# Performance work log

Hardware: AMD Instinct MI355X
Metric: run time of the kernel (lower is better)

The kernel has to match this reference:

```python
import jax, jax.numpy as jnp
import numpy as np

N_HEAD = 16
QK_NOPE = 128
QK_ROPE = 64
QK_HEAD = QK_NOPE + QK_ROPE  # 192
V_HEAD = 128
SCALE = 1.0 / np.sqrt(QK_HEAD)


def setup_inputs() -> dict:
    key = jax.random.key(0)
    ks = jax.random.split(key, 8)
    B, T, C = 2, 2048, 2048
    s = lambda fan: 1.0 / np.sqrt(fan)
    return {
        "x": jax.random.normal(ks[0], (B, T, C), jnp.float32),
        "freqs_cis": jax.random.uniform(ks[1], (T, QK_ROPE // 2, 2), jnp.float32),
        "w_q": jax.random.normal(ks[2], (C, N_HEAD * QK_HEAD), jnp.float32) * s(C),
        "w_kv_down": jax.random.normal(ks[3], (C, 256), jnp.float32) * s(C),
        "w_k_up": jax.random.normal(ks[4], (256, N_HEAD * QK_HEAD), jnp.float32) * s(256),
        "w_v_up": jax.random.normal(ks[5], (256, N_HEAD * V_HEAD), jnp.float32) * s(256),
        "w_o": jax.random.normal(ks[6], (N_HEAD * V_HEAD, C), jnp.float32) * s(N_HEAD * V_HEAD),
        "start_pos": 0,
    }


def _rotate_half(x):
    x1, x2 = x[..., : x.shape[-1] // 2], x[..., x.shape[-1] // 2 :]
    return jnp.concatenate([-x2, x1], axis=-1)


def reference(x, freqs_cis, w_q, w_kv_down, w_k_up, w_v_up, w_o, start_pos):
    B, T, C = x.shape
    # low-rank MLA projections
    q = (x @ w_q).reshape(B, T, N_HEAD, QK_HEAD)
    kv = x @ w_kv_down                                  # (B,T,r)
    k = (kv @ w_k_up).reshape(B, T, N_HEAD, QK_HEAD)
    v = (kv @ w_v_up).reshape(B, T, N_HEAD, V_HEAD)

    # inline RoPE on decoupled rope dims
    q_nope, q_rope = q[..., :QK_NOPE], q[..., QK_NOPE:]
    k_nope, k_rope = k[..., :QK_NOPE], k[..., QK_NOPE:]
    freqs = freqs_cis[start_pos : start_pos + T]         # (T, 32, 2)
    cos = freqs[..., 0][None, :, None, :]                # (1,T,1,32)
    sin = freqs[..., 1][None, :, None, :]
    rep = QK_ROPE // cos.shape[-1]
    cos = jnp.tile(cos, (1, 1, 1, rep))                  # (1,T,1,64)
    sin = jnp.tile(sin, (1, 1, 1, rep))
    q_rope = q_rope * cos + _rotate_half(q_rope) * sin
    k_rope = k_rope * cos + _rotate_half(k_rope) * sin
    q = jnp.concatenate([q_nope, q_rope], axis=-1)
    k = jnp.concatenate([k_nope, k_rope], axis=-1)

    # causal SDPA with mismatched QK vs V head dims
    scores = jnp.einsum("bqhd,bkhd->bhqk", q, k) * SCALE
    causal = jnp.tril(jnp.ones((T, T), dtype=bool))
    scores = jnp.where(causal[None, None], scores, -jnp.inf)
    probs = jax.nn.softmax(scores, axis=-1)
    out = jnp.einsum("bhqk,bkhd->bqhd", probs, v)        # (B,T,H,V_HEAD)
    out = out.reshape(B, T, N_HEAD * V_HEAD)
    return out @ w_o
```

## Files before the change

kernel.cpp:

```cpp
#include <hip/hip_runtime.h>
#include <stdint.h>

typedef unsigned short u16;
typedef float f32x4 __attribute__((ext_vector_type(4)));
typedef __bf16 bf16x8 __attribute__((ext_vector_type(8)));

static __device__ __forceinline__ u16 f2bf(float f) {
  union { float f; unsigned u; } v; v.f = f;
  unsigned r = v.u + 0x7fffu + ((v.u >> 16) & 1u);
  return (u16)(r >> 16);
}
static __device__ __forceinline__ float bf2f(u16 h) {
  union { unsigned u; float f; } v; v.u = ((unsigned)h) << 16;
  return v.f;
}

#define GLD_LDS16(gp, lp) __builtin_amdgcn_global_load_lds( \
    (__attribute__((address_space(1))) void*)(gp),          \
    (__attribute__((address_space(3))) void*)(lp), 16, 0, 0)

#define MFMA16(a, b, c) __builtin_amdgcn_mfma_f32_16x16x32_bf16((a), (b), (c), 0, 0, 0)

__global__ void conv_bf16_kernel(const float* __restrict__ in, u16* __restrict__ out, long n) {
  long stride = (long)gridDim.x * blockDim.x * 4;
  for (long i = ((long)blockIdx.x * blockDim.x + threadIdx.x) * 4; i < n; i += stride) {
    float4 v = *(const float4*)(in + i);
    union { u16 s[4]; uint2 u; } pk;
    pk.s[0] = f2bf(v.x); pk.s[1] = f2bf(v.y); pk.s[2] = f2bf(v.z); pk.s[3] = f2bf(v.w);
    *(uint2*)(out + i) = pk.u;
  }
}

__global__ void transpose_conv_kernel(const float* __restrict__ W, u16* __restrict__ WT,
                                      int K, int N) {
  __shared__ float tile[32][33];
  const int n0 = blockIdx.x * 32, k0 = blockIdx.y * 32;
  const int tx = threadIdx.x, ty = threadIdx.y;
#pragma unroll
  for (int i = 0; i < 32; i += 8) tile[ty + i][tx] = W[(long)(k0 + ty + i) * N + n0 + tx];
  __syncthreads();
#pragma unroll
  for (int i = 0; i < 32; i += 8)
    WT[(long)(n0 + ty + i) * K + k0 + tx] = f2bf(tile[tx][ty + i]);
}

template <bool OUT_F32>
__global__ __launch_bounds__(256, 2)
void gemm_bt_kernel(const u16* __restrict__ A, const u16* __restrict__ BT,
                    void* __restrict__ Cv, int N, int K, long sA, long sB, long sC) {
  const int bz = blockIdx.z;
  A += (long)bz * sA;
  BT += (long)bz * sB;
  const int m0 = blockIdx.y << 7, n0 = blockIdx.x << 7;
  __shared__ alignas(16) u16 lA[128 * 64];
  __shared__ alignas(16) u16 lB[128 * 64];
  const int tid = threadIdx.x;
  const int w = tid >> 6, l = tid & 63;
  const int wr = w >> 1, wc = w & 1;
  const int lrow = l & 15, lg = l >> 4;
  const int srow = l >> 3, scol = (l & 7) << 3;
  f32x4 acc[4][4] = {};
  for (int kt = 0; kt < K; kt += 64) {
    __syncthreads();
#pragma unroll
    for (int i = 0; i < 4; i++) {
      const int chunk = (w << 2) + i;
      const int row = (chunk << 3) + srow;
      GLD_LDS16(A + (long)(m0 + row) * K + kt + scol, &lA[chunk << 9]);
      GLD_LDS16(BT + (long)(n0 + row) * K + kt + scol, &lB[chunk << 9]);
    }
    __syncthreads();
#pragma unroll
    for (int kk = 0; kk < 2; kk++) {
      bf16x8 af[4], bb[4];
#pragma unroll
      for (int i = 0; i < 4; i++) {
        af[i] = *(const bf16x8*)&lA[((wr << 6) + (i << 4) + lrow) * 64 + (kk << 5) + (lg << 3)];
        bb[i] = *(const bf16x8*)&lB[((wc << 6) + (i << 4) + lrow) * 64 + (kk << 5) + (lg << 3)];
      }
#pragma unroll
      for (int mi = 0; mi < 4; mi++)
#pragma unroll
        for (int ni = 0; ni < 4; ni++)
          acc[mi][ni] = MFMA16(af[mi], bb[ni], acc[mi][ni]);
    }
  }
#pragma unroll
  for (int mi = 0; mi < 4; mi++) {
    const int r0 = m0 + (wr << 6) + (mi << 4) + (lg << 2);
#pragma unroll
    for (int ni = 0; ni < 4; ni++) {
      const int c0 = n0 + (wc << 6) + (ni << 4) + lrow;
#pragma unroll
      for (int r = 0; r < 4; r++) {
        const float val = acc[mi][ni][r];
        if constexpr (OUT_F32)
          ((float*)Cv + (long)bz * sC)[(long)(r0 + r) * N + c0] = val;
        else
          ((u16*)Cv + (long)bz * sC)[(long)(r0 + r) * N + c0] = f2bf(val);
      }
    }
  }
}

__global__ __launch_bounds__(256, 2)
void gemm_q_kvd_kernel(const u16* __restrict__ A, const u16* __restrict__ wqT,
                       const u16* __restrict__ wkdT, u16* __restrict__ qb,
                       u16* __restrict__ kvb) {
  constexpr int K = 2048;
  const int m0 = blockIdx.y << 7;
  const int n0raw = blockIdx.x << 7;
  const bool is_kv = n0raw >= 3072;
  const u16* BT = is_kv ? (wkdT + (long)(n0raw - 3072) * K) : (wqT + (long)n0raw * K);
  u16* C = is_kv ? kvb : qb;
  const int N = is_kv ? 256 : 3072;
  const int c_base = is_kv ? (n0raw - 3072) : n0raw;
  __shared__ alignas(16) u16 lA[128 * 64];
  __shared__ alignas(16) u16 lB[128 * 64];
  const int tid = threadIdx.x;
  const int w = tid >> 6, l = tid & 63;
  const int wr = w >> 1, wc = w & 1;
  const int lrow = l & 15, lg = l >> 4;
  const int srow = l >> 3, scol = (l & 7) << 3;
  f32x4 acc[4][4] = {};
  for (int kt = 0; kt < K; kt += 64) {
    __syncthreads();
#pragma unroll
    for (int i = 0; i < 4; i++) {
      const int chunk = (w << 2) + i;
      const int row = (chunk << 3) + srow;
      GLD_LDS16(A + (long)(m0 + row) * K + kt + scol, &lA[chunk << 9]);
      GLD_LDS16(BT + (long)row * K + kt + scol, &lB[chunk << 9]);
    }
    __syncthreads();
#pragma unroll
    for (int kk = 0; kk < 2; kk++) {
      bf16x8 af[4], bb[4];
#pragma unroll
      for (int i = 0; i < 4; i++) {
        af[i] = *(const bf16x8*)&lA[((wr << 6) + (i << 4) + lrow) * 64 + (kk << 5) + (lg << 3)];
        bb[i] = *(const bf16x8*)&lB[((wc << 6) + (i << 4) + lrow) * 64 + (kk << 5) + (lg << 3)];
      }
#pragma unroll
      for (int mi = 0; mi < 4; mi++)
#pragma unroll
        for (int ni = 0; ni < 4; ni++)
          acc[mi][ni] = MFMA16(af[mi], bb[ni], acc[mi][ni]);
    }
  }
#pragma unroll
  for (int mi = 0; mi < 4; mi++) {
    const int r0 = m0 + (wr << 6) + (mi << 4) + (lg << 2);
#pragma unroll
    for (int ni = 0; ni < 4; ni++) {
      const int c0 = c_base + (wc << 6) + (ni << 4) + lrow;
#pragma unroll
      for (int r = 0; r < 4; r++)
        C[(long)(r0 + r) * N + c0] = f2bf(acc[mi][ni][r]);
    }
  }
}

__global__ void rope_kernel(u16* __restrict__ q, u16* __restrict__ k,
                            const float* __restrict__ freqs, const int* __restrict__ sp_ptr) {
  const long idx = (long)blockIdx.x * blockDim.x + threadIdx.x;
  if (idx >= 2097152) return;
  const int i = (int)(idx & 31);
  const long r = idx >> 5;
  const int h = (int)(r & 15);
  const long bt = r >> 4;
  const int t = (int)(bt & 2047);
  const int sp = sp_ptr[0];
  const float c = freqs[((long)(sp + t) * 32 + i) * 2 + 0];
  const float s = freqs[((long)(sp + t) * 32 + i) * 2 + 1];
  const long base = bt * 3072 + h * 192 + 128;
  {
    float x1 = bf2f(q[base + i]), x2 = bf2f(q[base + i + 32]);
    q[base + i] = f2bf(x1 * c - x2 * s);
    q[base + i + 32] = f2bf(x2 * c + x1 * s);
  }
  {
    float x1 = bf2f(k[base + i]), x2 = bf2f(k[base + i + 32]);
    k[base + i] = f2bf(x1 * c - x2 * s);
    k[base + i + 32] = f2bf(x2 * c + x1 * s);
  }
}


__device__ __forceinline__ void attn_tile_step(
    const bf16x8* __restrict__ qf, f32x4* __restrict__ o, float* __restrict__ l_part,
    const int qrb, const int t0,
    const u16* __restrict__ Kl, const u16* __restrict__ Vl,
    u16* __restrict__ pw, const int lrow, const int lg) {
  constexpr float SCALE = 0.07216878364870323f;
  f32x4 s[4];
#pragma unroll
  for (int tb = 0; tb < 4; tb++) {
    f32x4 a = {};
#pragma unroll
    for (int kb = 0; kb < 6; kb++) {
      bf16x8 kf = *(const bf16x8*)&Kl[((tb << 4) + lrow) * 200 + (kb << 5) + (lg << 3)];
      a = MFMA16(qf[kb], kf, a);
    }
    s[tb] = a;
  }
#pragma unroll
  for (int tb = 0; tb < 4; tb++) {
    const int tt = t0 + (tb << 4) + lrow;
#pragma unroll
    for (int r = 0; r < 4; r++) {
      const int qrow = qrb + (lg << 2) + r;
      float p = __expf(s[tb][r] * SCALE);
      p = (tt <= qrow) ? p : 0.f;
      s[tb][r] = p;
      l_part[r] += p;
    }
  }
#pragma unroll
  for (int tb = 0; tb < 4; tb++)
#pragma unroll
    for (int r = 0; r < 4; r++)
      pw[((lg << 2) + r) * 68 + (tb << 4) + lrow] = f2bf(s[tb][r]);
  bf16x8 pf0 = *(const bf16x8*)&pw[lrow * 68 + (lg << 3)];
  bf16x8 pf1 = *(const bf16x8*)&pw[lrow * 68 + 32 + (lg << 3)];
#pragma unroll
  for (int db = 0; db < 8; db++) {
    bf16x8 v0 = *(const bf16x8*)&Vl[((db << 4) + lrow) * 72 + (lg << 3)];
    bf16x8 v1 = *(const bf16x8*)&Vl[((db << 4) + lrow) * 72 + 32 + (lg << 3)];
    o[db] = MFMA16(pf0, v0, o[db]);
    o[db] = MFMA16(pf1, v1, o[db]);
  }
}

__device__ __forceinline__ void attn_tile_step2(
    const bf16x8* __restrict__ qfA, const bf16x8* __restrict__ qfB,
    f32x4* __restrict__ oA, f32x4* __restrict__ oB,
    float* __restrict__ lpA, float* __restrict__ lpB,
    const int qrbA, const int qrbB, const int t0,
    const u16* __restrict__ Kl, const u16* __restrict__ Vl,
    u16* __restrict__ pwA, u16* __restrict__ pwB, const int lrow, const int lg) {
  constexpr float SCALE = 0.07216878364870323f;
  f32x4 sA[4], sB[4];
#pragma unroll
  for (int tb = 0; tb < 4; tb++) {
    f32x4 a = {}, bq = {};
#pragma unroll
    for (int kb = 0; kb < 6; kb++) {
      bf16x8 kf = *(const bf16x8*)&Kl[((tb << 4) + lrow) * 200 + (kb << 5) + (lg << 3)];
      a = MFMA16(qfA[kb], kf, a);
      bq = MFMA16(qfB[kb], kf, bq);
    }
    sA[tb] = a;
    sB[tb] = bq;
  }
#pragma unroll
  for (int tb = 0; tb < 4; tb++) {
    const int tt = t0 + (tb << 4) + lrow;
#pragma unroll
    for (int r = 0; r < 4; r++) {
      const int qrowA = qrbA + (lg << 2) + r;
      float pA = __expf(sA[tb][r] * SCALE);
      pA = (tt <= qrowA) ? pA : 0.f;
      sA[tb][r] = pA;
      lpA[r] += pA;
      const int qrowB = qrbB + (lg << 2) + r;
      float pB = __expf(sB[tb][r] * SCALE);
      pB = (tt <= qrowB) ? pB : 0.f;
      sB[tb][r] = pB;
      lpB[r] += pB;
    }
  }
#pragma unroll
  for (int tb = 0; tb < 4; tb++)
#pragma unroll
    for (int r = 0; r < 4; r++) {
      pwA[((lg << 2) + r) * 68 + (tb << 4) + lrow] = f2bf(sA[tb][r]);
      pwB[((lg << 2) + r) * 68 + (tb << 4) + lrow] = f2bf(sB[tb][r]);
    }
  bf16x8 pfA0 = *(const bf16x8*)&pwA[lrow * 68 + (lg << 3)];
  bf16x8 pfA1 = *(const bf16x8*)&pwA[lrow * 68 + 32 + (lg << 3)];
  bf16x8 pfB0 = *(const bf16x8*)&pwB[lrow * 68 + (lg << 3)];
  bf16x8 pfB1 = *(const bf16x8*)&pwB[lrow * 68 + 32 + (lg << 3)];
#pragma unroll
  for (int db = 0; db < 8; db++) {
    bf16x8 v0 = *(const bf16x8*)&Vl[((db << 4) + lrow) * 72 + (lg << 3)];
    bf16x8 v1 = *(const bf16x8*)&Vl[((db << 4) + lrow) * 72 + 32 + (lg << 3)];
    oA[db] = MFMA16(pfA0, v0, oA[db]);
    oB[db] = MFMA16(pfB0, v0, oB[db]);
    oA[db] = MFMA16(pfA1, v1, oA[db]);
    oB[db] = MFMA16(pfB1, v1, oB[db]);
  }
}

__device__ __forceinline__ void attn_write(
    u16* __restrict__ ob, const f32x4* __restrict__ o, const float* __restrict__ l_part,
    const int lrow, const int lg) {
#pragma unroll
  for (int r = 0; r < 4; r++) {
    float l = l_part[r];
#pragma unroll
    for (int d = 1; d < 16; d <<= 1) l += __shfl_xor(l, d);
    const float inv = 1.f / l;
#pragma unroll
    for (int db = 0; db < 8; db++)
      ob[(long)((lg << 2) + r) * 2048 + (db << 4) + lrow] = f2bf(o[db][r] * inv);
  }
}

__global__ __launch_bounds__(256, 2)
void attn_kernel(const u16* __restrict__ q, const u16* __restrict__ k,
                 const u16* __restrict__ vT, u16* __restrict__ out) {
  const int bid = blockIdx.x;
  const int xcd = bid & 7;
  const int rest = bid >> 3;
  const int pair = rest & 15;
  const int bh = ((rest >> 4) << 3) | xcd;
  const int b = bh >> 4, h = bh & 15;
  const int tid = threadIdx.x, w = tid >> 6, l = tid & 63;
  const int lrow = l & 15, lg = l >> 4;
  const int qtA = pair, qtB = 31 - pair;
  const int qrbA = (qtA << 6) + (w << 4);
  const int qrbB = (qtB << 6) + (w << 4);
  __shared__ alignas(16) u16 Kl[64 * 200];
  __shared__ alignas(16) u16 Vl[128 * 72];
  __shared__ alignas(16) u16 Pl[4][2][16 * 68];

  bf16x8 qfA[6], qfB[6];
  {
    const u16* qbA = q + ((long)b * 2048 + qrbA + lrow) * 3072 + h * 192;
    const u16* qbB = q + ((long)b * 2048 + qrbB + lrow) * 3072 + h * 192;
#pragma unroll
    for (int kb = 0; kb < 6; kb++) {
      qfA[kb] = *(const bf16x8*)&qbA[(kb << 5) + (lg << 3)];
      qfB[kb] = *(const bf16x8*)&qbB[(kb << 5) + (lg << 3)];
    }
  }
  f32x4 oA[8] = {}, oB[8] = {};
  float lA[4] = {}, lB[4] = {};

  const u16* kbh = k + (long)b * 2048 * 3072 + h * 192;
  const u16* vbh = vT + ((long)b * 2048 + h * 128) * 2048;
  const int tEndA = qtA << 6, tEndB = qtB << 6;

  for (int t0 = 0; t0 <= tEndB; t0 += 64) {
    __syncthreads();
#pragma unroll
    for (int i = 0; i < 6; i++) {
      int c = (i << 8) + tid;
      int row = c / 24, col = (c % 24) << 3;
      *(bf16x8*)&Kl[row * 200 + col] = *(const bf16x8*)&kbh[(long)(t0 + row) * 3072 + col];
    }
#pragma unroll
    for (int i = 0; i < 4; i++) {
      int c = (i << 8) + tid;
      int row = c >> 3, col = (c & 7) << 3;
      *(bf16x8*)&Vl[row * 72 + col] = *(const bf16x8*)&vbh[(long)row * 2048 + t0 + col];
    }
    __syncthreads();
    if (t0 <= tEndA)
      attn_tile_step2(qfA, qfB, oA, oB, lA, lB, qrbA, qrbB, t0, Kl, Vl,
                      &Pl[w][0][0], &Pl[w][1][0], lrow, lg);
    else
      attn_tile_step(qfB, oB, lB, qrbB, t0, Kl, Vl, &Pl[w][1][0], lrow, lg);
  }
  attn_write(out + ((long)b * 2048 + qrbA) * 2048 + (h << 7), oA, lA, lrow, lg);
  attn_write(out + ((long)b * 2048 + qrbB) * 2048 + (h << 7), oB, lB, lrow, lg);
}

extern "C" void kernel_launch(void* const* d_in, const int* in_sizes, int n_in,
                              void* d_out, int out_size, void* d_ws, size_t ws_size,
                              hipStream_t stream) {
  const float* x = (const float*)d_in[0];
  const float* fcis = (const float*)d_in[1];
  const float* w_q = (const float*)d_in[2];
  const float* w_kvd = (const float*)d_in[3];
  const float* w_ku = (const float*)d_in[4];
  const float* w_vu = (const float*)d_in[5];
  const float* w_o = (const float*)d_in[6];
  const int* start_pos = (const int*)d_in[7];
  float* out = (float*)d_out;

  char* p = (char*)d_ws;
  auto alloc = [&](long bytes) -> char* {
    char* r = p;
    p += (bytes + 255) & ~255ll;
    return r;
  };
  u16* xb = (u16*)alloc(4096ll * 2048 * 2);
  u16* wqT = (u16*)alloc(3072ll * 2048 * 2);
  u16* wkdT = (u16*)alloc(256ll * 2048 * 2);
  u16* wkuT = (u16*)alloc(3072ll * 256 * 2);
  u16* wvuT = (u16*)alloc(2048ll * 256 * 2);
  u16* woT = (u16*)alloc(2048ll * 2048 * 2);
  u16* qb = (u16*)alloc(4096ll * 3072 * 2);
  u16* kvb = (u16*)alloc(4096ll * 256 * 2);
  u16* kb = (u16*)alloc(4096ll * 3072 * 2);
  u16* aob = (u16*)alloc(4096ll * 2048 * 2);
  u16* vTb = xb;

  conv_bf16_kernel<<<2048, 256, 0, stream>>>(x, xb, 4096ll * 2048);
  dim3 tb(32, 8);
  transpose_conv_kernel<<<dim3(3072 / 32, 2048 / 32), tb, 0, stream>>>(w_q, wqT, 2048, 3072);
  transpose_conv_kernel<<<dim3(256 / 32, 2048 / 32), tb, 0, stream>>>(w_kvd, wkdT, 2048, 256);
  transpose_conv_kernel<<<dim3(3072 / 32, 256 / 32), tb, 0, stream>>>(w_ku, wkuT, 256, 3072);
  transpose_conv_kernel<<<dim3(2048 / 32, 256 / 32), tb, 0, stream>>>(w_vu, wvuT, 256, 2048);
  transpose_conv_kernel<<<dim3(2048 / 32, 2048 / 32), tb, 0, stream>>>(w_o, woT, 2048, 2048);

  gemm_q_kvd_kernel<<<dim3(26, 32), 256, 0, stream>>>(xb, wqT, wkdT, qb, kvb);
  gemm_bt_kernel<false><<<dim3(24, 32, 1), 256, 0, stream>>>(kvb, wkuT, kb, 3072, 256, 0, 0, 0);
  gemm_bt_kernel<false><<<dim3(16, 16, 2), 256, 0, stream>>>(wvuT, kvb, vTb, 2048, 256,
                                                             0, 2048ll * 256, 2048ll * 2048);
  rope_kernel<<<8192, 256, 0, stream>>>(qb, kb, fcis, start_pos);
  attn_kernel<<<512, 256, 0, stream>>>(qb, kb, vTb, aob);
  gemm_bt_kernel<true><<<dim3(16, 32, 1), 256, 0, stream>>>(aob, woT, out, 2048, 2048, 0, 0, 0);
}
```

Measured before the change: 301.1 us.

## Merge K/V up-projection GEMMs and widen attention blocks to share K/V tiles

The two up-projection GEMMs (K and transposed V) are merged into one launch whose grid covers both problems, which saves a launch and lets the two fill the GPU together. The attention kernel moves from 256 to 512 threads per block. Each block now handles two query-tile pairs, so every K/V tile loaded into LDS serves twice as many query rows and global K/V traffic is halved. The trade-off is fewer blocks (256), a larger LDS footprint, and some wavefronts sitting idle during the tail iterations that only the longer pair needs.

```diff
diff --git a/kernel.cpp b/kernel.cpp
--- a/kernel.cpp
+++ b/kernel.cpp
@@ -161,6 +161,72 @@
   }
 }
 
+__global__ __launch_bounds__(256, 2)
+void gemm_kup_vt_kernel(const u16* __restrict__ kvb, const u16* __restrict__ wkuT,
+                        const u16* __restrict__ wvuT, u16* __restrict__ kb,
+                        u16* __restrict__ vTb) {
+  constexpr int K = 256;
+  const int bid = blockIdx.x;
+  const u16 *A, *BT;
+  u16* C;
+  int N, m0, n0;
+  if (bid < 768) {
+    A = kvb; BT = wkuT; C = kb; N = 3072;
+    m0 = (bid / 24) << 7; n0 = (bid % 24) << 7;
+  } else {
+    int r = bid - 768;
+    const int bz = r >> 8;
+    r &= 255;
+    A = wvuT; BT = kvb + (long)bz * 2048 * 256; C = vTb + (long)bz * 2048 * 2048;
+    N = 2048;
+    m0 = (r >> 4) << 7; n0 = (r & 15) << 7;
+  }
+  __shared__ alignas(16) u16 lA[128 * 64];
+  __shared__ alignas(16) u16 lB[128 * 64];
+  const int tid = threadIdx.x;
+  const int w = tid >> 6, l = tid & 63;
+  const int wr = w >> 1, wc = w & 1;
+  const int lrow = l & 15, lg = l >> 4;
+  const int srow = l >> 3, scol = (l & 7) << 3;
+  f32x4 acc[4][4] = {};
+  for (int kt = 0; kt < K; kt += 64) {
+    __syncthreads();
+#pragma unroll
+    for (int i = 0; i < 4; i++) {
+      const int chunk = (w << 2) + i;
+      const int row = (chunk << 3) + srow;
+      GLD_LDS16(A + (long)(m0 + row) * K + kt + scol, &lA[chunk << 9]);
+      GLD_LDS16(BT + (long)(n0 + row) * K + kt + scol, &lB[chunk << 9]);
+    }
+    __syncthreads();
+#pragma unroll
+    for (int kk = 0; kk < 2; kk++) {
+      bf16x8 af[4], bb[4];
+#pragma unroll
+      for (int i = 0; i < 4; i++) {
+        af[i] = *(const bf16x8*)&lA[((wr << 6) + (i << 4) + lrow) * 64 + (kk << 5) + (lg << 3)];
+        bb[i] = *(const bf16x8*)&lB[((wc << 6) + (i << 4) + lrow) * 64 + (kk << 5) + (lg << 3)];
+      }
+#pragma unroll
+      for (int mi = 0; mi < 4; mi++)
+#pragma unroll
+        for (int ni = 0; ni < 4; ni++)
+          acc[mi][ni] = MFMA16(af[mi], bb[ni], acc[mi][ni]);
+    }
+  }
+#pragma unroll
+  for (int mi = 0; mi < 4; mi++) {
+    const int r0 = m0 + (wr << 6) + (mi << 4) + (lg << 2);
+#pragma unroll
+    for (int ni = 0; ni < 4; ni++) {
+      const int c0 = n0 + (wc << 6) + (ni << 4) + lrow;
+#pragma unroll
+      for (int r = 0; r < 4; r++)
+        C[(long)(r0 + r) * N + c0] = f2bf(acc[mi][ni][r]);
+    }
+  }
+}
+
 __global__ void rope_kernel(u16* __restrict__ q, u16* __restrict__ k,
                             const float* __restrict__ freqs, const int* __restrict__ sp_ptr) {
   const long idx = (long)blockIdx.x * blockDim.x + threadIdx.x;
@@ -307,23 +373,25 @@
   }
 }
 
-__global__ __launch_bounds__(256, 2)
+__global__ __launch_bounds__(512, 4)
 void attn_kernel(const u16* __restrict__ q, const u16* __restrict__ k,
                  const u16* __restrict__ vT, u16* __restrict__ out) {
   const int bid = blockIdx.x;
   const int xcd = bid & 7;
   const int rest = bid >> 3;
-  const int pair = rest & 15;
-  const int bh = ((rest >> 4) << 3) | xcd;
+  const int pair = rest & 7;
+  const int bh = ((rest >> 3) << 3) | xcd;
   const int b = bh >> 4, h = bh & 15;
   const int tid = threadIdx.x, w = tid >> 6, l = tid & 63;
+  const int g = w >> 2;
   const int lrow = l & 15, lg = l >> 4;
-  const int qtA = pair, qtB = 31 - pair;
-  const int qrbA = (qtA << 6) + (w << 4);
-  const int qrbB = (qtB << 6) + (w << 4);
+  const int qtA = (pair << 1) + g;
+  const int qtB = 31 - (pair << 1) - g;
+  const int qrbA = (qtA << 6) + ((w & 3) << 4);
+  const int qrbB = (qtB << 6) + ((w & 3) << 4);
   __shared__ alignas(16) u16 Kl[64 * 200];
   __shared__ alignas(16) u16 Vl[128 * 72];
-  __shared__ alignas(16) u16 Pl[4][2][16 * 68];
+  __shared__ alignas(16) u16 Pl[8][2][16 * 68];
 
   bf16x8 qfA[6], qfB[6];
   {
@@ -341,18 +409,19 @@
   const u16* kbh = k + (long)b * 2048 * 3072 + h * 192;
   const u16* vbh = vT + ((long)b * 2048 + h * 128) * 2048;
   const int tEndA = qtA << 6, tEndB = qtB << 6;
-
-  for (int t0 = 0; t0 <= tEndB; t0 += 64) {
-    __syncthreads();
-#pragma unroll
-    for (int i = 0; i < 6; i++) {
-      int c = (i << 8) + tid;
+  const int tEndMax = (31 - (pair << 1)) << 6;
+
+  for (int t0 = 0; t0 <= tEndMax; t0 += 64) {
+    __syncthreads();
+#pragma unroll
+    for (int i = 0; i < 3; i++) {
+      int c = (i << 9) + tid;
       int row = c / 24, col = (c % 24) << 3;
       *(bf16x8*)&Kl[row * 200 + col] = *(const bf16x8*)&kbh[(long)(t0 + row) * 3072 + col];
     }
 #pragma unroll
-    for (int i = 0; i < 4; i++) {
-      int c = (i << 8) + tid;
+    for (int i = 0; i < 2; i++) {
+      int c = (i << 9) + tid;
       int row = c >> 3, col = (c & 7) << 3;
       *(bf16x8*)&Vl[row * 72 + col] = *(const bf16x8*)&vbh[(long)row * 2048 + t0 + col];
     }
@@ -360,7 +429,7 @@
     if (t0 <= tEndA)
       attn_tile_step2(qfA, qfB, oA, oB, lA, lB, qrbA, qrbB, t0, Kl, Vl,
                       &Pl[w][0][0], &Pl[w][1][0], lrow, lg);
-    else
+    else if (t0 <= tEndB)
       attn_tile_step(qfB, oB, lB, qrbB, t0, Kl, Vl, &Pl[w][1][0], lrow, lg);
   }
   attn_write(out + ((long)b * 2048 + qrbA) * 2048 + (h << 7), oA, lA, lrow, lg);
@@ -407,10 +476,8 @@
   transpose_conv_kernel<<<dim3(2048 / 32, 2048 / 32), tb, 0, stream>>>(w_o, woT, 2048, 2048);
 
   gemm_q_kvd_kernel<<<dim3(26, 32), 256, 0, stream>>>(xb, wqT, wkdT, qb, kvb);
-  gemm_bt_kernel<false><<<dim3(24, 32, 1), 256, 0, stream>>>(kvb, wkuT, kb, 3072, 256, 0, 0, 0);
-  gemm_bt_kernel<false><<<dim3(16, 16, 2), 256, 0, stream>>>(wvuT, kvb, vTb, 2048, 256,
-                                                             0, 2048ll * 256, 2048ll * 2048);
+  gemm_kup_vt_kernel<<<1280, 256, 0, stream>>>(kvb, wkuT, wvuT, kb, vTb);
   rope_kernel<<<8192, 256, 0, stream>>>(qb, kb, fcis, start_pos);
-  attn_kernel<<<512, 256, 0, stream>>>(qb, kb, vTb, aob);
+  attn_kernel<<<256, 512, 0, stream>>>(qb, kb, vTb, aob);
   gemm_bt_kernel<true><<<dim3(16, 32, 1), 256, 0, stream>>>(aob, woT, out, 2048, 2048, 0, 0, 0);
 }
```

Result: slower. 399.4 us (+32.7%).
